# Kernel tuning notes

Measured on AMD Instinct MI355X. Metric: run time of the kernel, lower is better.

Reference implementation:

```python
import jax, jax.numpy as jnp
import numpy as np

N, E, NFEAT, HID, HEADS, NCLASS = 100000, 1600000, 256, 64, 1, 32


def gat_conv(x, src, dst, W, a_src, a_dst, b, H, C, concat):
    n = x.shape[0]
    h = (x @ W).reshape(n, H, C)                      # [N,H,C]
    a_s = (h * a_src).sum(-1)                          # [N,H]
    a_d = (h * a_dst).sum(-1)                          # [N,H]
    e = jax.nn.leaky_relu(a_s[src] + a_d[dst], 0.2)    # [E,H]
    emax = jax.ops.segment_max(e, dst, num_segments=n)
    emax = jnp.where(jnp.isfinite(emax), emax, 0.0)
    ex = jnp.exp(e - emax[dst])
    denom = jax.ops.segment_sum(ex, dst, num_segments=n)
    alpha = ex / (denom[dst] + 1e-16)                  # segment softmax over in-edges of dst
    msg = h[src] * alpha[:, :, None]                   # [E,H,C]
    out = jax.ops.segment_sum(msg, dst, num_segments=n)
    out = out.reshape(n, H * C) if concat else out.mean(axis=1)
    return out + b


def setup_inputs() -> dict:
    key = jax.random.key(0)
    ks = jax.random.split(key, 14)
    x = jax.random.normal(ks[0], (N, NFEAT), dtype=jnp.float32)
    edge_index = jax.random.randint(ks[1], (2, E), 0, N, dtype=jnp.int64)
    s = 0.05
    return {
        'x': x, 'edge_index': edge_index,
        'W1': jax.random.normal(ks[2], (NFEAT, HEADS * HID), jnp.float32) * s,
        'as1': jax.random.normal(ks[3], (HEADS, HID), jnp.float32) * s,
        'ad1': jax.random.normal(ks[4], (HEADS, HID), jnp.float32) * s,
        'b1': jnp.zeros((HEADS * HID,), jnp.float32),
        'W2': jax.random.normal(ks[5], (HEADS * HID, HEADS * HID), jnp.float32) * s,
        'as2': jax.random.normal(ks[6], (HEADS, HID), jnp.float32) * s,
        'ad2': jax.random.normal(ks[7], (HEADS, HID), jnp.float32) * s,
        'b2': jnp.zeros((HEADS * HID,), jnp.float32),
        'W3': jax.random.normal(ks[8], (HEADS * HID, HEADS * NCLASS), jnp.float32) * s,
        'as3': jax.random.normal(ks[9], (HEADS, NCLASS), jnp.float32) * s,
        'ad3': jax.random.normal(ks[10], (HEADS, NCLASS), jnp.float32) * s,
        'b3': jnp.zeros((NCLASS,), jnp.float32),
    }


def reference(x, edge_index, W1, as1, ad1, b1, W2, as2, ad2, b2, W3, as3, ad3, b3):
    # add self loops (PyG GATConv add_self_loops=True)
    loop = jnp.arange(N, dtype=edge_index.dtype)
    src = jnp.concatenate([edge_index[0], loop])
    dst = jnp.concatenate([edge_index[1], loop])
    out = jax.nn.leaky_relu(gat_conv(x, src, dst, W1, as1, ad1, b1, HEADS, HID, True), 0.01)
    out = jax.nn.leaky_relu(gat_conv(out, src, dst, W2, as2, ad2, b2, HEADS, HID, True), 0.01)
    out = gat_conv(out, src, dst, W3, as3, ad3, b3, HEADS, NCLASS, False)
    return out
```

## Files before the change

### kernel.cpp

```cpp
#include <hip/hip_runtime.h>

#define NN 100000
#define NE 1600000
#define NF 256
#define HD 64
#define NC 32

#define BKS 8
#define NBK ((NN + 255) >> 8)
#define CHUNK 4096
#define NBLK ((NE + CHUNK - 1) / CHUNK)

__device__ __forceinline__ float lrelu02(float x) { return fmaxf(x, 0.2f * x); }

typedef __attribute__((ext_vector_type(8))) short bf16x8;
typedef __attribute__((ext_vector_type(4))) float f32x4;
typedef __attribute__((ext_vector_type(8))) _Float16 f16x8;

__device__ __forceinline__ unsigned short f2bf(float f) {
    unsigned int u = __float_as_uint(f);
    unsigned int r = u + 0x7FFFu + ((u >> 16) & 1u);
    return (unsigned short)(r >> 16);
}
__device__ __forceinline__ float bf2f(unsigned short s) {
    return __uint_as_float(((unsigned int)s) << 16);
}


__global__ __launch_bounds__(256) void bucket_hist(const int* __restrict__ dst, int* __restrict__ gcnt) {
    __shared__ int hist[NBK];
    int tid = threadIdx.x;
    for (int i = tid; i < NBK; i += 256) hist[i] = 0;
    __syncthreads();
    int base = blockIdx.x * CHUNK;
    #pragma unroll
    for (int k = 0; k < CHUNK / 256; k++) {
        int i = base + k * 256 + tid;
        if (i < NE) atomicAdd(&hist[dst[i] >> BKS], 1);
    }
    __syncthreads();
    for (int i = tid; i < NBK; i += 256) if (hist[i]) atomicAdd(&gcnt[i], hist[i]);
}

__global__ void bucket_scan(const int* __restrict__ gcnt, int* __restrict__ gbase, int* __restrict__ gcur) {
    __shared__ int sh[512];
    int tid = threadIdx.x;
    int v = (tid < NBK) ? gcnt[tid] : 0;
    sh[tid] = v;
    __syncthreads();
    for (int d = 1; d < 512; d <<= 1) {
        int t = (tid >= d) ? sh[tid - d] : 0;
        __syncthreads();
        sh[tid] += t;
        __syncthreads();
    }
    if (tid < NBK) { int ex = sh[tid] - v; gbase[tid] = ex; gcur[tid] = ex; }
}

__global__ __launch_bounds__(256) void bin_edges(const int* __restrict__ src, const int* __restrict__ dst,
                                                 int* __restrict__ gcur, unsigned int* __restrict__ ebuf) {
    __shared__ int hist[NBK];
    __shared__ int excl[NBK];
    __shared__ int runbase[NBK];
    __shared__ int ssum[256];
    __shared__ unsigned int sorted[CHUNK];
    __shared__ unsigned short sortedb[CHUNK];
    int tid = threadIdx.x;
    int base = blockIdx.x * CHUNK;
    int n = NE - base; if (n > CHUNK) n = CHUNK;

    for (int i = tid; i < NBK; i += 256) hist[i] = 0;
    __syncthreads();

    unsigned int pk[CHUNK / 256];
    int bk[CHUNK / 256];
    #pragma unroll
    for (int k = 0; k < CHUNK / 256; k++) {
        int i = base + k * 256 + tid;
        if (i < NE) {
            int s = src[i], d = dst[i];
            pk[k] = ((unsigned int)s << 8) | ((unsigned int)d & 255u);
            bk[k] = d >> BKS;
            atomicAdd(&hist[bk[k]], 1);
        } else bk[k] = -1;
    }
    __syncthreads();
    int h0 = (2 * tid < NBK) ? hist[2 * tid] : 0;
    int h1 = (2 * tid + 1 < NBK) ? hist[2 * tid + 1] : 0;
    ssum[tid] = h0 + h1;
    __syncthreads();
    for (int d = 1; d < 256; d <<= 1) {
        int t = (tid >= d) ? ssum[tid - d] : 0;
        __syncthreads();
        ssum[tid] += t;
        __syncthreads();
    }
    int pref = ssum[tid] - (h0 + h1);
    if (2 * tid < NBK) excl[2 * tid] = pref;
    if (2 * tid + 1 < NBK) excl[2 * tid + 1] = pref + h0;
    for (int b = tid; b < NBK; b += 256) {
        int c = hist[b];
        runbase[b] = c ? atomicAdd(&gcur[b], c) : 0;
    }
    __syncthreads();
    #pragma unroll
    for (int k = 0; k < CHUNK / 256; k++) {
        if (bk[k] >= 0) {
            int r = atomicAdd(&excl[bk[k]], 1);
            sorted[r] = pk[k];
            sortedb[r] = (unsigned short)bk[k];
        }
    }
    __syncthreads();
    for (int i = tid; i < n; i += 256) {
        int b = sortedb[i];
        int local_rank = i - (excl[b] - hist[b]);
        ebuf[runbase[b] + local_rank] = sorted[i];
    }
}

__global__ __launch_bounds__(256) void bucket_csr(const unsigned int* __restrict__ ebuf, const int* __restrict__ gbase,
                                                  const int* __restrict__ gcnt,
                                                  int* __restrict__ offs, int* __restrict__ csr) {
    __shared__ int hist[256], cur[256], ssum[256];
    int b = blockIdx.x, tid = threadIdx.x;
    int ebeg = gbase[b], cnt = gcnt[b];
    int node0 = b << BKS;
    hist[tid] = 0;
    __syncthreads();
    for (int i = ebeg + tid; i < ebeg + cnt; i += 256)
        atomicAdd(&hist[ebuf[i] & 255u], 1);
    __syncthreads();
    int v = hist[tid];
    ssum[tid] = v;
    __syncthreads();
    for (int d = 1; d < 256; d <<= 1) {
        int t = (tid >= d) ? ssum[tid - d] : 0;
        __syncthreads();
        ssum[tid] += t;
        __syncthreads();
    }
    int ex = ebeg + ssum[tid] - v;
    cur[tid] = ex;
    int nnode = NN - node0; if (nnode > 256) nnode = 256;
    if (tid < nnode) offs[node0 + tid] = ex;
    if (b == NBK - 1 && tid == nnode - 1) offs[NN] = ebeg + cnt;
    __syncthreads();
    for (int i = ebeg + tid; i < ebeg + cnt; i += 256) {
        unsigned int e = ebuf[i];
        int pos = atomicAdd(&cur[e & 255u], 1);
        csr[pos] = (int)(e >> 8);
    }
}


template <int CIN, int COUT>
__global__ __launch_bounds__(128) void mfma_gemm(const float* __restrict__ in, const float* __restrict__ W,
                                                 const float* __restrict__ a_s, const float* __restrict__ a_d,
                                                 _Float16* __restrict__ hout, float* __restrict__ asv,
                                                 float* __restrict__ adv) {
    const int KC  = 32;
    const int BM  = 64;
    const int NCT = COUT / 16;
    const int NCH = CIN / KC;
    const int SPT = (4 * COUT) / 128;

    __shared__ unsigned short Bh[2][4 * COUT * 8];
    __shared__ unsigned short Bl[2][4 * COUT * 8];

    int tid  = threadIdx.x;
    int lane = tid & 63;
    int wave = tid >> 6;
    int fr = lane & 15;
    int kg = lane >> 4;
    int n0base = blockIdx.x * BM;
    int rbase  = n0base + wave * 32;

    int scol[SPT], skg[SPT];
    #pragma unroll
    for (int i = 0; i < SPT; i++) {
        int s = tid + i * 128;
        scol[i] = s % COUT;
        skg[i]  = s / COUT;
    }

    float4 xr[4];
    float  wv[SPT][8];
    bf16x8 ah[2], al[2];

    f32x4 acc[2][NCT];
    #pragma unroll
    for (int rt = 0; rt < 2; rt++)
        #pragma unroll
        for (int ct = 0; ct < NCT; ct++) acc[rt][ct] = (f32x4){0.f, 0.f, 0.f, 0.f};

    auto load_A = [&](int k0) {
        #pragma unroll
        for (int rt = 0; rt < 2; rt++) {
            int gr = rbase + rt * 16 + fr;
            if (gr < NN) {
                const float* p = &in[(size_t)gr * CIN + k0 + kg * 8];
                xr[rt * 2 + 0] = *(const float4*)p;
                xr[rt * 2 + 1] = *(const float4*)(p + 4);
            } else {
                xr[rt * 2 + 0] = make_float4(0.f, 0.f, 0.f, 0.f);
                xr[rt * 2 + 1] = make_float4(0.f, 0.f, 0.f, 0.f);
            }
        }
    };
    auto conv_A = [&]() {
        #pragma unroll
        for (int rt = 0; rt < 2; rt++) {
            const float* v = (const float*)&xr[rt * 2];
            unsigned short hs[8], ls[8];
            #pragma unroll
            for (int j = 0; j < 8; j++) {
                hs[j] = f2bf(v[j]);
                ls[j] = f2bf(v[j] - bf2f(hs[j]));
            }
            ah[rt] = *(bf16x8*)hs;
            al[rt] = *(bf16x8*)ls;
        }
    };
    auto load_B = [&](int k0) {
        #pragma unroll
        for (int i = 0; i < SPT; i++)
            #pragma unroll
            for (int j = 0; j < 8; j++)
                wv[i][j] = W[(size_t)(k0 + skg[i] * 8 + j) * COUT + scol[i]];
    };
    auto write_B = [&](int buf) {
        #pragma unroll
        for (int i = 0; i < SPT; i++) {
            unsigned short hs[8], ls[8];
            #pragma unroll
            for (int j = 0; j < 8; j++) {
                hs[j] = f2bf(wv[i][j]);
                ls[j] = f2bf(wv[i][j] - bf2f(hs[j]));
            }
            int idx = (skg[i] * COUT + scol[i]) * 8;
            *(uint4*)&Bh[buf][idx] = *(uint4*)hs;
            *(uint4*)&Bl[buf][idx] = *(uint4*)ls;
        }
    };
    auto do_mfma = [&](int buf) {
        #pragma unroll
        for (int ct = 0; ct < NCT; ct++) {
            int col = ct * 16 + fr;
            bf16x8 bh = *(const bf16x8*)&Bh[buf][(kg * COUT + col) * 8];
            bf16x8 bl = *(const bf16x8*)&Bl[buf][(kg * COUT + col) * 8];
            #pragma unroll
            for (int rt = 0; rt < 2; rt++) {
                acc[rt][ct] = __builtin_amdgcn_mfma_f32_16x16x32_bf16(ah[rt], bh, acc[rt][ct], 0, 0, 0);
                acc[rt][ct] = __builtin_amdgcn_mfma_f32_16x16x32_bf16(ah[rt], bl, acc[rt][ct], 0, 0, 0);
                acc[rt][ct] = __builtin_amdgcn_mfma_f32_16x16x32_bf16(al[rt], bh, acc[rt][ct], 0, 0, 0);
            }
        }
    };

    load_A(0);
    load_B(0);
    conv_A();
    write_B(0);
    __syncthreads();

    for (int t = 0; t < NCH; t++) {
        int cur = t & 1;
        if (t + 1 < NCH) {
            load_A((t + 1) * KC);
            load_B((t + 1) * KC);
        }
        do_mfma(cur);
        if (t + 1 < NCH) {
            write_B(cur ^ 1);
            conv_A();
            __syncthreads();
        }
    }

    float As_l[NCT], Ad_l[NCT];
    #pragma unroll
    for (int ct = 0; ct < NCT; ct++) {
        As_l[ct] = a_s[ct * 16 + fr];
        Ad_l[ct] = a_d[ct * 16 + fr];
    }
    #pragma unroll
    for (int rt = 0; rt < 2; rt++) {
        #pragma unroll
        for (int r = 0; r < 4; r++) {
            int row = rbase + rt * 16 + kg * 4 + r;
            if (row < NN) {
                #pragma unroll
                for (int ct = 0; ct < NCT; ct++)
                    hout[(size_t)row * COUT + ct * 16 + fr] = (_Float16)acc[rt][ct][r];
            }
            float ps = 0.f, pd = 0.f;
            #pragma unroll
            for (int ct = 0; ct < NCT; ct++) {
                ps += acc[rt][ct][r] * As_l[ct];
                pd += acc[rt][ct][r] * Ad_l[ct];
            }
            #pragma unroll
            for (int off = 1; off < 16; off <<= 1) {
                ps += __shfl_xor(ps, off);
                pd += __shfl_xor(pd, off);
            }
            if (fr == 0 && row < NN) { asv[row] = ps; adv[row] = pd; }
        }
    }
}


template <int C, bool ACT>
__global__ __launch_bounds__(256) void gat_agg(const _Float16* __restrict__ h16, const float* __restrict__ asv,
                                               const float* __restrict__ adv, const int* __restrict__ offs,
                                               const int* __restrict__ csr,
                                               const float* __restrict__ bias, float* __restrict__ out) {
    const int LR = C / 8;
    const int G  = 64 / LR;
    const f16x8* hh = (const f16x8*)h16;
    int lane = threadIdx.x & 63;
    int v = blockIdx.x * 4 + (threadIdx.x >> 6);
    int beg = offs[v], end = offs[v + 1];
    int g = lane / LR, r = lane % LR;
    float adv_v = adv[v];

    float acc[8] = {0.f, 0.f, 0.f, 0.f, 0.f, 0.f, 0.f, 0.f};
    float dsum = 0.f;
    #pragma unroll 4
    for (int e = beg + g; e < end; e += G) {
        int s = csr[e];
        float ww = __expf(lrelu02(asv[s] + adv_v));
        f16x8 hv = hh[(size_t)s * LR + r];
        dsum += ww;
        #pragma unroll
        for (int j = 0; j < 8; j++) acc[j] += ww * (float)hv[j];
    }
    #pragma unroll
    for (int off = LR; off < 64; off <<= 1) {
        #pragma unroll
        for (int j = 0; j < 8; j++) acc[j] += __shfl_xor(acc[j], off);
        dsum += __shfl_xor(dsum, off);
    }
    if (g == 0) {
        float selfw = __expf(lrelu02(asv[v] + adv_v));
        f16x8 hs = hh[(size_t)v * LR + r];
        #pragma unroll
        for (int j = 0; j < 8; j++) acc[j] += selfw * (float)hs[j];
        dsum += selfw;
        float inv = 1.f / (dsum + 1e-16f);
        float4 bb0 = ((const float4*)bias)[r * 2];
        float4 bb1 = ((const float4*)bias)[r * 2 + 1];
        float4 o0, o1;
        o0.x = acc[0] * inv + bb0.x; o0.y = acc[1] * inv + bb0.y;
        o0.z = acc[2] * inv + bb0.z; o0.w = acc[3] * inv + bb0.w;
        o1.x = acc[4] * inv + bb1.x; o1.y = acc[5] * inv + bb1.y;
        o1.z = acc[6] * inv + bb1.z; o1.w = acc[7] * inv + bb1.w;
        if (ACT) {
            o0.x = fmaxf(o0.x, 0.01f * o0.x); o0.y = fmaxf(o0.y, 0.01f * o0.y);
            o0.z = fmaxf(o0.z, 0.01f * o0.z); o0.w = fmaxf(o0.w, 0.01f * o0.w);
            o1.x = fmaxf(o1.x, 0.01f * o1.x); o1.y = fmaxf(o1.y, 0.01f * o1.y);
            o1.z = fmaxf(o1.z, 0.01f * o1.z); o1.w = fmaxf(o1.w, 0.01f * o1.w);
        }
        ((float4*)out)[(size_t)v * (C / 4) + r * 2]     = o0;
        ((float4*)out)[(size_t)v * (C / 4) + r * 2 + 1] = o1;
    }
}


extern "C" void kernel_launch(void* const* d_in, const int* in_sizes, int n_in,
                              void* d_out, int out_size, void* d_ws, size_t ws_size,
                              hipStream_t stream) {
    const float* x   = (const float*)d_in[0];
    const int*   ei  = (const int*)d_in[1];
    const float* W1  = (const float*)d_in[2];
    const float* as1 = (const float*)d_in[3];
    const float* ad1 = (const float*)d_in[4];
    const float* b1  = (const float*)d_in[5];
    const float* W2  = (const float*)d_in[6];
    const float* as2 = (const float*)d_in[7];
    const float* ad2 = (const float*)d_in[8];
    const float* b2  = (const float*)d_in[9];
    const float* W3  = (const float*)d_in[10];
    const float* as3 = (const float*)d_in[11];
    const float* ad3 = (const float*)d_in[12];
    const float* b3  = (const float*)d_in[13];
    float* out = (float*)d_out;

    const int* srcp = ei;
    const int* dstp = ei + NE;

    char* w = (char*)d_ws;
    _Float16* h16 = (_Float16*)w;  w += sizeof(_Float16) * (size_t)NN * HD;
    float* featB = (float*)w;   w += sizeof(float) * (size_t)NN * HD;
    float* asv   = (float*)w;   w += sizeof(float) * NN;
    float* advv  = (float*)w;   w += sizeof(float) * NN;
    int* offs    = (int*)w;     w += sizeof(int) * (NN + 1);
    int* csr     = (int*)w;     w += sizeof(int) * (size_t)NE;
    unsigned int* ebuf = (unsigned int*)w; w += sizeof(unsigned int) * (size_t)NE;
    int* gcnt    = (int*)w;     w += sizeof(int) * NBK;
    int* gbase   = (int*)w;     w += sizeof(int) * NBK;
    int* gcur    = (int*)w;     w += sizeof(int) * NBK;

    const int GBM = (NN + 63) / 64;

    hipMemsetAsync(gcnt, 0, sizeof(int) * NBK, stream);
    bucket_hist<<<NBLK, 256, 0, stream>>>(dstp, gcnt);
    bucket_scan<<<1, 512, 0, stream>>>(gcnt, gbase, gcur);
    bin_edges<<<NBLK, 256, 0, stream>>>(srcp, dstp, gcur, ebuf);
    bucket_csr<<<NBK, 256, 0, stream>>>(ebuf, gbase, gcnt, offs, csr);

    mfma_gemm<NF, HD><<<GBM, 128, 0, stream>>>(x, W1, as1, ad1, h16, asv, advv);
    gat_agg<HD, true><<<NN / 4, 256, 0, stream>>>(h16, asv, advv, offs, csr, b1, featB);

    mfma_gemm<HD, HD><<<GBM, 128, 0, stream>>>(featB, W2, as2, ad2, h16, asv, advv);
    gat_agg<HD, true><<<NN / 4, 256, 0, stream>>>(h16, asv, advv, offs, csr, b2, featB);

    mfma_gemm<HD, NC><<<GBM, 128, 0, stream>>>(featB, W3, as3, ad3, h16, asv, advv);
    gat_agg<NC, false><<<NN / 4, 256, 0, stream>>>(h16, asv, advv, offs, csr, b3, out);
}
```

Before: 423.9 us.

## Replace bucketed two-pass CSR build with direct per-node atomic counting sort

Replaces the bucket histogram, local binning and per-bucket CSR kernels with a simpler counting sort. A per-node histogram built with global atomics feeds a three-stage prefix scan, and a final scatter places edges with per-node atomic cursors. This removes the intermediate ebuf pass and the shared-memory sorting, but relies on 1.6M scattered global atomics with random access, which may contend. The order of edges within each node is now nondeterministic, which can change floating-point summation order.

```diff
diff --git a/kernel.cpp b/kernel.cpp
--- a/kernel.cpp
+++ b/kernel.cpp
@@ -6,10 +6,7 @@
 #define HD 64
 #define NC 32
 
-#define BKS 8
 #define NBK ((NN + 255) >> 8)
-#define CHUNK 4096
-#define NBLK ((NE + CHUNK - 1) / CHUNK)
 
 __device__ __forceinline__ float lrelu02(float x) { return fmaxf(x, 0.2f * x); }
 
@@ -27,25 +24,33 @@
 }
 
 
-__global__ __launch_bounds__(256) void bucket_hist(const int* __restrict__ dst, int* __restrict__ gcnt) {
-    __shared__ int hist[NBK];
-    int tid = threadIdx.x;
-    for (int i = tid; i < NBK; i += 256) hist[i] = 0;
+__global__ __launch_bounds__(256) void node_hist(const int* __restrict__ dst, int* __restrict__ dcount) {
+    int i = blockIdx.x * 256 + threadIdx.x;
+    if (i < NE) atomicAdd(&dcount[dst[i]], 1);
+}
+
+__global__ __launch_bounds__(256) void scan_local(const int* __restrict__ dcount,
+                                                  int* __restrict__ lexcl, int* __restrict__ psum) {
+    __shared__ int sh[256];
+    int b = blockIdx.x, tid = threadIdx.x;
+    int i = b * 256 + tid;
+    int v = (i < NN) ? dcount[i] : 0;
+    sh[tid] = v;
     __syncthreads();
-    int base = blockIdx.x * CHUNK;
-    #pragma unroll
-    for (int k = 0; k < CHUNK / 256; k++) {
-        int i = base + k * 256 + tid;
-        if (i < NE) atomicAdd(&hist[dst[i] >> BKS], 1);
-    }
-    __syncthreads();
-    for (int i = tid; i < NBK; i += 256) if (hist[i]) atomicAdd(&gcnt[i], hist[i]);
-}
-
-__global__ void bucket_scan(const int* __restrict__ gcnt, int* __restrict__ gbase, int* __restrict__ gcur) {
+    for (int d = 1; d < 256; d <<= 1) {
+        int t = (tid >= d) ? sh[tid - d] : 0;
+        __syncthreads();
+        sh[tid] += t;
+        __syncthreads();
+    }
+    if (i < NN) lexcl[i] = sh[tid] - v;
+    if (tid == 255) psum[b] = sh[255];
+}
+
+__global__ void scan_block(const int* __restrict__ psum, int* __restrict__ pbase) {
     __shared__ int sh[512];
     int tid = threadIdx.x;
-    int v = (tid < NBK) ? gcnt[tid] : 0;
+    int v = (tid < NBK) ? psum[tid] : 0;
     sh[tid] = v;
     __syncthreads();
     for (int d = 1; d < 512; d <<= 1) {
@@ -54,102 +59,26 @@
         sh[tid] += t;
         __syncthreads();
     }
-    if (tid < NBK) { int ex = sh[tid] - v; gbase[tid] = ex; gcur[tid] = ex; }
-}
-
-__global__ __launch_bounds__(256) void bin_edges(const int* __restrict__ src, const int* __restrict__ dst,
-                                                 int* __restrict__ gcur, unsigned int* __restrict__ ebuf) {
-    __shared__ int hist[NBK];
-    __shared__ int excl[NBK];
-    __shared__ int runbase[NBK];
-    __shared__ int ssum[256];
-    __shared__ unsigned int sorted[CHUNK];
-    __shared__ unsigned short sortedb[CHUNK];
-    int tid = threadIdx.x;
-    int base = blockIdx.x * CHUNK;
-    int n = NE - base; if (n > CHUNK) n = CHUNK;
-
-    for (int i = tid; i < NBK; i += 256) hist[i] = 0;
-    __syncthreads();
-
-    unsigned int pk[CHUNK / 256];
-    int bk[CHUNK / 256];
-    #pragma unroll
-    for (int k = 0; k < CHUNK / 256; k++) {
-        int i = base + k * 256 + tid;
-        if (i < NE) {
-            int s = src[i], d = dst[i];
-            pk[k] = ((unsigned int)s << 8) | ((unsigned int)d & 255u);
-            bk[k] = d >> BKS;
-            atomicAdd(&hist[bk[k]], 1);
-        } else bk[k] = -1;
-    }
-    __syncthreads();
-    int h0 = (2 * tid < NBK) ? hist[2 * tid] : 0;
-    int h1 = (2 * tid + 1 < NBK) ? hist[2 * tid + 1] : 0;
-    ssum[tid] = h0 + h1;
-    __syncthreads();
-    for (int d = 1; d < 256; d <<= 1) {
-        int t = (tid >= d) ? ssum[tid - d] : 0;
-        __syncthreads();
-        ssum[tid] += t;
-        __syncthreads();
-    }
-    int pref = ssum[tid] - (h0 + h1);
-    if (2 * tid < NBK) excl[2 * tid] = pref;
-    if (2 * tid + 1 < NBK) excl[2 * tid + 1] = pref + h0;
-    for (int b = tid; b < NBK; b += 256) {
-        int c = hist[b];
-        runbase[b] = c ? atomicAdd(&gcur[b], c) : 0;
-    }
-    __syncthreads();
-    #pragma unroll
-    for (int k = 0; k < CHUNK / 256; k++) {
-        if (bk[k] >= 0) {
-            int r = atomicAdd(&excl[bk[k]], 1);
-            sorted[r] = pk[k];
-            sortedb[r] = (unsigned short)bk[k];
-        }
-    }
-    __syncthreads();
-    for (int i = tid; i < n; i += 256) {
-        int b = sortedb[i];
-        int local_rank = i - (excl[b] - hist[b]);
-        ebuf[runbase[b] + local_rank] = sorted[i];
-    }
-}
-
-__global__ __launch_bounds__(256) void bucket_csr(const unsigned int* __restrict__ ebuf, const int* __restrict__ gbase,
-                                                  const int* __restrict__ gcnt,
-                                                  int* __restrict__ offs, int* __restrict__ csr) {
-    __shared__ int hist[256], cur[256], ssum[256];
-    int b = blockIdx.x, tid = threadIdx.x;
-    int ebeg = gbase[b], cnt = gcnt[b];
-    int node0 = b << BKS;
-    hist[tid] = 0;
-    __syncthreads();
-    for (int i = ebeg + tid; i < ebeg + cnt; i += 256)
-        atomicAdd(&hist[ebuf[i] & 255u], 1);
-    __syncthreads();
-    int v = hist[tid];
-    ssum[tid] = v;
-    __syncthreads();
-    for (int d = 1; d < 256; d <<= 1) {
-        int t = (tid >= d) ? ssum[tid - d] : 0;
-        __syncthreads();
-        ssum[tid] += t;
-        __syncthreads();
-    }
-    int ex = ebeg + ssum[tid] - v;
-    cur[tid] = ex;
-    int nnode = NN - node0; if (nnode > 256) nnode = 256;
-    if (tid < nnode) offs[node0 + tid] = ex;
-    if (b == NBK - 1 && tid == nnode - 1) offs[NN] = ebeg + cnt;
-    __syncthreads();
-    for (int i = ebeg + tid; i < ebeg + cnt; i += 256) {
-        unsigned int e = ebuf[i];
-        int pos = atomicAdd(&cur[e & 255u], 1);
-        csr[pos] = (int)(e >> 8);
+    if (tid < NBK) pbase[tid] = sh[tid] - v;
+}
+
+__global__ __launch_bounds__(256) void scan_final(const int* __restrict__ lexcl, const int* __restrict__ pbase,
+                                                  int* __restrict__ offs, int* __restrict__ cur) {
+    int i = blockIdx.x * 256 + threadIdx.x;
+    if (i < NN) {
+        int o = lexcl[i] + pbase[i >> 8];
+        offs[i] = o;
+        cur[i]  = o;
+    }
+    if (i == NN) offs[NN] = NE;
+}
+
+__global__ __launch_bounds__(256) void edge_scatter(const int* __restrict__ src, const int* __restrict__ dst,
+                                                    int* __restrict__ cur, int* __restrict__ csr) {
+    int i = blockIdx.x * 256 + threadIdx.x;
+    if (i < NE) {
+        int pos = atomicAdd(&cur[dst[i]], 1);
+        csr[pos] = src[i];
     }
 }
 
@@ -397,18 +326,21 @@
     float* advv  = (float*)w;   w += sizeof(float) * NN;
     int* offs    = (int*)w;     w += sizeof(int) * (NN + 1);
     int* csr     = (int*)w;     w += sizeof(int) * (size_t)NE;
-    unsigned int* ebuf = (unsigned int*)w; w += sizeof(unsigned int) * (size_t)NE;
-    int* gcnt    = (int*)w;     w += sizeof(int) * NBK;
-    int* gbase   = (int*)w;     w += sizeof(int) * NBK;
-    int* gcur    = (int*)w;     w += sizeof(int) * NBK;
+    int* dcount  = (int*)w;     w += sizeof(int) * NN;
+    int* lexcl   = (int*)w;     w += sizeof(int) * NN;
+    int* curp    = (int*)w;     w += sizeof(int) * NN;
+    int* psum    = (int*)w;     w += sizeof(int) * NBK;
+    int* pbase   = (int*)w;     w += sizeof(int) * NBK;
 
     const int GBM = (NN + 63) / 64;
-
-    hipMemsetAsync(gcnt, 0, sizeof(int) * NBK, stream);
-    bucket_hist<<<NBLK, 256, 0, stream>>>(dstp, gcnt);
-    bucket_scan<<<1, 512, 0, stream>>>(gcnt, gbase, gcur);
-    bin_edges<<<NBLK, 256, 0, stream>>>(srcp, dstp, gcur, ebuf);
-    bucket_csr<<<NBK, 256, 0, stream>>>(ebuf, gbase, gcnt, offs, csr);
+    const int GBE = (NE + 255) / 256;
+
+    hipMemsetAsync(dcount, 0, sizeof(int) * NN, stream);
+    node_hist<<<GBE, 256, 0, stream>>>(dstp, dcount);
+    scan_local<<<NBK, 256, 0, stream>>>(dcount, lexcl, psum);
+    scan_block<<<1, 512, 0, stream>>>(psum, pbase);
+    scan_final<<<NBK + 1, 256, 0, stream>>>(lexcl, pbase, offs, curp);
+    edge_scatter<<<GBE, 256, 0, stream>>>(srcp, dstp, curp, csr);
 
     mfma_gemm<NF, HD><<<GBM, 128, 0, stream>>>(x, W1, as1, ad1, h16, asv, advv);
     gat_agg<HD, true><<<NN / 4, 256, 0, stream>>>(h16, asv, advv, offs, csr, b1, featB);
```

After: 554.0 us. 1.31x slower.
